# Optimization experiments

Hardware: AMD Instinct MI355X
Metric: run time of the kernel (lower is better)

Reference implementation:

```python
import jax, jax.numpy as jnp
import numpy as np
import math

D_MODEL = 512
N_HEADS = 8
FACTOR = 5
B, L = 2, 2048


def setup_inputs() -> dict:
    key = jax.random.key(0)
    ks = jax.random.split(key, 10)
    s = 1.0 / math.sqrt(D_MODEL)
    inp = {
        "x": jax.random.normal(ks[0], (B, L, D_MODEL), dtype=jnp.float32),
        "samp_idx": jax.random.randint(ks[1], (FACTOR * L,), 0, L),
        "Wq": jax.random.normal(ks[2], (D_MODEL, D_MODEL), dtype=jnp.float32) * s,
        "bq": jnp.zeros((D_MODEL,), dtype=jnp.float32),
        "Wk": jax.random.normal(ks[3], (D_MODEL, D_MODEL), dtype=jnp.float32) * s,
        "bk": jnp.zeros((D_MODEL,), dtype=jnp.float32),
        "Wv": jax.random.normal(ks[4], (D_MODEL, D_MODEL), dtype=jnp.float32) * s,
        "bv": jnp.zeros((D_MODEL,), dtype=jnp.float32),
        "Wo": jax.random.normal(ks[5], (D_MODEL, D_MODEL), dtype=jnp.float32) * s,
        "bo": jnp.zeros((D_MODEL,), dtype=jnp.float32),
    }
    return inp


def reference(x, Wq, bq, Wk, bk, Wv, bv, Wo, bo, samp_idx):
    B_, L_, D = x.shape
    H = N_HEADS
    dk = D // H
    scale = 1.0 / math.sqrt(dk)

    def proj(W, b):
        # torch Linear: x @ W.T + b, then split heads -> [B, H, L, dk]
        y = jnp.einsum('bld,ed->ble', x, W) + b
        return y.reshape(B_, L_, H, dk).transpose(0, 2, 1, 3)

    q = proj(Wq, bq)
    k = proj(Wk, bk)
    v = proj(Wv, bv)

    # _prob_QK: random key sampling (shared indices across B, H)
    K_sample = k[:, :, samp_idx, :]                       # [B, H, factor*L, dk]
    QKs = jnp.einsum('bhle,bhse->bhls', q, K_sample) * scale  # [B, H, L, factor*L]
    M = QKs.max(-1) - QKs.mean(-1)                        # [B, H, L]
    U = jnp.argmax(M, axis=-1)                            # [B, H] -- single query per head

    # gather the selected query per (b, h): [B, H, 1, dk]
    q_red = jnp.take_along_axis(q, U[:, :, None, None], axis=2)

    scores = jnp.einsum('bhle,bhse->bhls', q_red, k) * scale  # [B, H, 1, L]
    attn = jax.nn.softmax(scores, axis=-1)
    context = jnp.einsum('bhls,bhse->bhle', attn, v)          # [B, H, 1, dk]

    # expand to all query positions, merge heads
    context = jnp.broadcast_to(context, (B_, H, L_, dk))
    context = context.transpose(0, 2, 1, 3).reshape(B_, L_, D)
    return jnp.einsum('bld,ed->ble', context, Wo) + bo
```

## Files before the change

kernel.cpp:

```cpp
#include <hip/hip_runtime.h>

#define B_ 2
#define L_ 2048
#define D_ 512
#define H_ 8
#define DK 64
#define S_ 10240
#define SCALE 0.125f

#define QSZ (4096 * 512)

typedef _Float16 f16;
typedef __attribute__((ext_vector_type(8))) _Float16 f16x8;
typedef __attribute__((ext_vector_type(4))) float f32x4;

#define AS1 __attribute__((address_space(1)))
#define AS3 __attribute__((address_space(3)))

__global__ __launch_bounds__(256) void prep_kernel(
    const float* __restrict__ x,
    const float* __restrict__ Wq, const float* __restrict__ Wk,
    const float* __restrict__ bq, const float* __restrict__ bk,
    const int* __restrict__ samp,
    f16* __restrict__ xh, f16* __restrict__ xl,
    f16* __restrict__ wh, f16* __restrict__ wl,
    float* __restrict__ biascat, int* __restrict__ counts,
    float* __restrict__ xbc_part)
{
    const int bid = blockIdx.x;
    const int t = threadIdx.x;
    if (bid < 1024) {
        const size_t i0 = ((size_t)bid * 256 + t) * 8;
        const float4 a = *(const float4*)&x[i0];
        const float4 b = *(const float4*)&x[i0 + 4];
        const float vals[8] = {a.x, a.y, a.z, a.w, b.x, b.y, b.z, b.w};
        union { f16 h[8]; uint4 u; } H, Lo;
#pragma unroll
        for (int j = 0; j < 8; j++) {
            const f16 hh = (f16)vals[j];
            H.h[j] = hh;
            Lo.h[j] = (f16)(vals[j] - (float)hh);
        }
        *(uint4*)&xh[i0] = H.u;
        *(uint4*)&xl[i0] = Lo.u;
    } else if (bid < 1280) {
        const size_t i0 = ((size_t)(bid - 1024) * 256 + t) * 8;
        const float* src = (i0 < (size_t)512 * 512) ? Wq + i0
                                                    : Wk + (i0 - (size_t)512 * 512);
        const float4 a = *(const float4*)&src[0];
        const float4 b = *(const float4*)&src[4];
        const float vals[8] = {a.x, a.y, a.z, a.w, b.x, b.y, b.z, b.w};
        union { f16 h[8]; uint4 u; } H, Lo;
#pragma unroll
        for (int j = 0; j < 8; j++) {
            const f16 hh = (f16)vals[j];
            H.h[j] = hh;
            Lo.h[j] = (f16)(vals[j] - (float)hh);
        }
        *(uint4*)&wh[i0] = H.u;
        *(uint4*)&wl[i0] = Lo.u;
        if (bid == 1024)
            for (int e = t; e < 1024; e += 256)
                biascat[e] = (e < 512) ? bq[e] : bk[e - 512];
    } else if (bid < 1344) {
        const int p = bid - 1280;
        const int bb = p >> 5, chunk = p & 31;
        const int s0 = chunk * 320;
        float ax = 0.f, ay = 0.f;
        const float* xb = x + (size_t)bb * L_ * D_ + t * 2;
        for (int i = 0; i < 320; i++) {
            const int j = samp[s0 + i];
            const float2 v = *(const float2*)(xb + (size_t)j * D_);
            ax += v.x; ay += v.y;
        }
        float2 st; st.x = ax; st.y = ay;
        *(float2*)&xbc_part[((size_t)(bb * 32 + chunk)) * 512 + t * 2] = st;
    } else {
        int4 z; z.x = 0; z.y = 0; z.z = 0; z.w = 0;
        ((int4*)counts)[(bid - 1344) * 256 + t] = z;
    }
}

__global__ __launch_bounds__(256) void projqk_kernel(
    const f16* __restrict__ xh, const f16* __restrict__ xl,
    const f16* __restrict__ wh, const f16* __restrict__ wl,
    const float* __restrict__ biascat,
    const float* __restrict__ xbc_part, const float* __restrict__ Wk,
    const float* __restrict__ bk, const int* __restrict__ samp,
    int* __restrict__ counts, float* __restrict__ kbar,
    f16* __restrict__ qh, f16* __restrict__ ql,
    f16* __restrict__ kh, f16* __restrict__ kl)
{
    const int bid = blockIdx.x;
    const int t = threadIdx.x;

    __shared__ __align__(16) f16 lds[24576];

    if (bid >= 512) {
        const int bh = bid - 512;
        const int b = bh >> 3, h = bh & 7;
        float* xc = (float*)lds;

        for (int i = bh * 640 + t; i < (bh + 1) * 640; i += 256)
            atomicAdd(&counts[samp[i]], 1);

        float ax = 0.f, ay = 0.f;
#pragma unroll
        for (int p = 0; p < 32; p++) {
            const float2 v = *(const float2*)&xbc_part[((size_t)(b * 32 + p)) * 512 + t * 2];
            ax += v.x; ay += v.y;
        }
        xc[t * 2]     = ax * (1.0f / (float)S_);
        xc[t * 2 + 1] = ay * (1.0f / (float)S_);
        __syncthreads();

        const int row = t >> 2, quarter = t & 3;
        const float* wr = Wk + (size_t)(h * 64 + row) * 512 + quarter * 128;
        float s = 0.f;
#pragma unroll 8
        for (int d = 0; d < 32; d++) {
            const float4 w4 = *(const float4*)&wr[d * 4];
            const int xo = quarter * 128 + d * 4;
            s += w4.x * xc[xo] + w4.y * xc[xo + 1] + w4.z * xc[xo + 2] + w4.w * xc[xo + 3];
        }
        s += __shfl_xor(s, 1);
        s += __shfl_xor(s, 2);
        if (quarter == 0) kbar[bh * 64 + row] = s + bk[h * 64 + row];
        return;
    }

    const int n0 = (bid & 63) * 64;
    const int e0 = (bid >> 6) * 128;

    f16* ash = lds;
    f16* asl = lds + 4096;
    f16* bsh = lds + 8192;
    f16* bsl = lds + 16384;

    const int lane = t & 63, wid = t >> 6;
    const int wr = wid >> 1, wc = wid & 1;
    const int lrow = lane & 15, lk = lane >> 4;
    const int srw = lane >> 3;
    const int scg = (lane & 7) ^ srw;

    f32x4 acc[2][4];
#pragma unroll
    for (int i = 0; i < 2; i++)
#pragma unroll
        for (int j = 0; j < 4; j++)
#pragma unroll
            for (int r = 0; r < 4; r++) acc[i][j][r] = 0.f;

    for (int kt = 0; kt < 8; kt++) {
        __syncthreads();
#pragma unroll
        for (int i_ = 0; i_ < 2; i_++) {
            const int chunk = wid * 2 + i_;
            const int row = chunk * 8 + srw;
            const size_t goa = (size_t)(n0 + row) * 512 + kt * 64 + scg * 8;
            __builtin_amdgcn_global_load_lds((const AS1 void*)(xh + goa),
                                             (AS3 void*)(&ash[chunk * 512]), 16, 0, 0);
            __builtin_amdgcn_global_load_lds((const AS1 void*)(xl + goa),
                                             (AS3 void*)(&asl[chunk * 512]), 16, 0, 0);
        }
#pragma unroll
        for (int i_ = 0; i_ < 4; i_++) {
            const int chunk = wid * 4 + i_;
            const int row = chunk * 8 + srw;
            const size_t gob = (size_t)(e0 + row) * 512 + kt * 64 + scg * 8;
            __builtin_amdgcn_global_load_lds((const AS1 void*)(wh + gob),
                                             (AS3 void*)(&bsh[chunk * 512]), 16, 0, 0);
            __builtin_amdgcn_global_load_lds((const AS1 void*)(wl + gob),
                                             (AS3 void*)(&bsl[chunk * 512]), 16, 0, 0);
        }
        __syncthreads();

#pragma unroll
        for (int kk = 0; kk < 2; kk++) {
            f16x8 ah[2], al[2], bh_[4], bl_[4];
#pragma unroll
            for (int lt = 0; lt < 2; lt++) {
                const int row = wr * 32 + lt * 16 + lrow;
                const int cs = (kk * 4 + lk) ^ (row & 7);
                const int o = row * 64 + cs * 8;
                ah[lt] = *(const f16x8*)&ash[o];
                al[lt] = *(const f16x8*)&asl[o];
            }
#pragma unroll
            for (int jt = 0; jt < 4; jt++) {
                const int row = wc * 64 + jt * 16 + lrow;
                const int cs = (kk * 4 + lk) ^ (row & 7);
                const int o = row * 64 + cs * 8;
                bh_[jt] = *(const f16x8*)&bsh[o];
                bl_[jt] = *(const f16x8*)&bsl[o];
            }
#pragma unroll
            for (int lt = 0; lt < 2; lt++)
#pragma unroll
                for (int jt = 0; jt < 4; jt++) {
                    acc[lt][jt] = __builtin_amdgcn_mfma_f32_16x16x32_f16(
                        ah[lt], bh_[jt], acc[lt][jt], 0, 0, 0);
                    acc[lt][jt] = __builtin_amdgcn_mfma_f32_16x16x32_f16(
                        ah[lt], bl_[jt], acc[lt][jt], 0, 0, 0);
                    acc[lt][jt] = __builtin_amdgcn_mfma_f32_16x16x32_f16(
                        al[lt], bh_[jt], acc[lt][jt], 0, 0, 0);
                }
        }
    }

    const int PSTR = 72;
    f16* tile = lds + wid * 32 * PSTR;
    const int ebase = e0 + wc * 64;
    const bool isQ = ((bid >> 6) < 4);
    const int colbase = ((bid >> 6) & 3) * 128;

#pragma unroll
    for (int round = 0; round < 2; round++) {
        __syncthreads();
#pragma unroll
        for (int jt = 0; jt < 4; jt++) {
            const float bval = biascat[ebase + jt * 16 + lrow];
#pragma unroll
            for (int lt = 0; lt < 2; lt++)
#pragma unroll
                for (int r = 0; r < 4; r++) {
                    const float y = acc[lt][jt][r] + bval;
                    const f16 hi = (f16)y;
                    const f16 val = (round == 0) ? hi : (f16)(y - (float)hi);
                    tile[(lt * 16 + lk * 4 + r) * PSTR + jt * 16 + lrow] = val;
                }
        }
        __syncthreads();
        f16* dst = isQ ? ((round == 0) ? qh : ql) : ((round == 0) ? kh : kl);
        for (int i = t; i < 1024; i += 256) {
            const int row = i >> 4, cc = i & 15;
            const int swid = (row >> 5) * 2 + (cc >> 3);
            const int trow = row & 31, tcol = (cc & 7) * 8;
            const int n = n0 + row;
            const int col = colbase + cc * 8;
            *(uint4*)&dst[(size_t)n * 512 + col] =
                *(const uint4*)&lds[swid * 32 * PSTR + trow * PSTR + tcol];
        }
    }
}

__global__ __launch_bounds__(256, 2) void mstat_kernel(
    const f16* __restrict__ qh, const f16* __restrict__ ql,
    const f16* __restrict__ kh, const f16* __restrict__ kl,
    const int* __restrict__ counts, const float* __restrict__ kbar,
    float* __restrict__ bestv, int* __restrict__ besti)
{
    const int id = blockIdx.x;
    const int xcd = id & 7, seq = id >> 3;
    const int bh = xcd * 2 + (seq >> 5);
    const int inner = seq & 31;
    const int lt16 = inner >> 1;
    const int js = inner & 1;
    const int jbase = js * 8;
    const int b = bh >> 3, h = bh & 7;
    const int l0 = lt16 * 128;
    const int t = threadIdx.x;
    const int lane = t & 63, wid = t >> 6;
    const int wr = wid >> 1, wc = wid & 1;
    const int lrow = lane & 15, lk = lane >> 4;

    __shared__ __align__(16) f16 kbuf[2][2][128 * 64];
    __shared__ float kbar_lds[64];
    __shared__ float dot_lds[128];
    __shared__ float wv_[4];
    __shared__ int wi_[4];

    f16x8 qa_h[2][4], qa_l[2][4];
    {
        const size_t qrowbase = (size_t)(b * L_ + l0 + wr * 64) * D_ + h * DK;
#pragma unroll
        for (int kk = 0; kk < 2; kk++)
#pragma unroll
            for (int lt = 0; lt < 4; lt++) {
                const size_t o = qrowbase + (size_t)(lt * 16 + lrow) * D_ + kk * 32 + lk * 8;
                qa_h[kk][lt] = *(const f16x8*)&qh[o];
                qa_l[kk][lt] = *(const f16x8*)&ql[o];
            }
    }
    if (t < 64) kbar_lds[t] = kbar[bh * 64 + t];

    const f16* khb = kh + (size_t)b * L_ * D_ + h * DK;
    const f16* klb = kl + (size_t)b * L_ * D_ + h * DK;

    const int srw = lane >> 3;
    const int scg = (lane & 7) ^ srw;
#define STAGE_TILE(jt, nb)                                                     \
    {                                                                          \
        const size_t gb0 = (size_t)((jt) * 128) * D_;                          \
        _Pragma("unroll")                                                      \
        for (int i_ = 0; i_ < 4; i_++) {                                       \
            const int chunk = wid * 4 + i_;                                    \
            const size_t go = gb0 + (size_t)(chunk * 8 + srw) * D_ + scg * 8;  \
            __builtin_amdgcn_global_load_lds(                                  \
                (const AS1 void*)(khb + go),                                   \
                (AS3 void*)(&kbuf[nb][0][chunk * 512]), 16, 0, 0);             \
            __builtin_amdgcn_global_load_lds(                                  \
                (const AS1 void*)(klb + go),                                   \
                (AS3 void*)(&kbuf[nb][1][chunk * 512]), 16, 0, 0);             \
        }                                                                      \
    }

    STAGE_TILE(jbase, 0)
    __syncthreads();

    float rmax[4][4];
#pragma unroll
    for (int lt = 0; lt < 4; lt++)
#pragma unroll
        for (int r = 0; r < 4; r++) rmax[lt][r] = -3.9e38f;

    int cur = 0;
    for (int jj = 0; jj < 8; jj++) {
        const int jt = jbase + jj;
        if (jj < 7) STAGE_TILE(jt + 1, cur ^ 1)

        f32x4 acc[4][4];
#pragma unroll
        for (int i = 0; i < 4; i++)
#pragma unroll
            for (int j = 0; j < 4; j++)
#pragma unroll
                for (int r = 0; r < 4; r++) acc[i][j][r] = 0.f;

#pragma unroll
        for (int kk = 0; kk < 2; kk++) {
            f16x8 bhf[4], blf[4];
#pragma unroll
            for (int jtt = 0; jtt < 4; jtt++) {
                const int row = wc * 64 + jtt * 16 + lrow;
                const int cs = (kk * 4 + lk) ^ (row & 7);
                const int o = row * 64 + cs * 8;
                bhf[jtt] = *(const f16x8*)&kbuf[cur][0][o];
                blf[jtt] = *(const f16x8*)&kbuf[cur][1][o];
            }
#pragma unroll
            for (int lt = 0; lt < 4; lt++)
#pragma unroll
                for (int jtt = 0; jtt < 4; jtt++) {
                    acc[lt][jtt] = __builtin_amdgcn_mfma_f32_16x16x32_f16(
                        qa_h[kk][lt], bhf[jtt], acc[lt][jtt], 0, 0, 0);
                    acc[lt][jtt] = __builtin_amdgcn_mfma_f32_16x16x32_f16(
                        qa_h[kk][lt], blf[jtt], acc[lt][jtt], 0, 0, 0);
                    acc[lt][jtt] = __builtin_amdgcn_mfma_f32_16x16x32_f16(
                        qa_l[kk][lt], bhf[jtt], acc[lt][jtt], 0, 0, 0);
                }
        }

#pragma unroll
        for (int jtt = 0; jtt < 4; jtt++) {
            const int cj = jt * 128 + wc * 64 + jtt * 16 + lrow;
            const float addend = (counts[cj] > 0) ? 0.f : -3.0e38f;
#pragma unroll
            for (int lt = 0; lt < 4; lt++)
#pragma unroll
                for (int r = 0; r < 4; r++)
                    rmax[lt][r] = fmaxf(rmax[lt][r], acc[lt][jtt][r] + addend);
        }

        __syncthreads();
        cur ^= 1;
    }

#pragma unroll
    for (int m = 1; m < 16; m <<= 1)
#pragma unroll
        for (int lt = 0; lt < 4; lt++)
#pragma unroll
            for (int r = 0; r < 4; r++)
                rmax[lt][r] = fmaxf(rmax[lt][r], __shfl_xor(rmax[lt][r], m));

    {
        float dlt[4];
#pragma unroll
        for (int lt = 0; lt < 4; lt++) {
            float d = 0.f;
#pragma unroll
            for (int kk = 0; kk < 2; kk++) {
                const f16x8 hv = qa_h[kk][lt];
                const f16x8 lv = qa_l[kk][lt];
#pragma unroll
                for (int i = 0; i < 8; i++)
                    d += ((float)hv[i] + (float)lv[i]) * kbar_lds[kk * 32 + lk * 8 + i];
            }
            dlt[lt] = d;
        }
#pragma unroll
        for (int lt = 0; lt < 4; lt++) {
            dlt[lt] += __shfl_xor(dlt[lt], 16);
            dlt[lt] += __shfl_xor(dlt[lt], 32);
        }
        if (lane < 16) {
#pragma unroll
            for (int lt = 0; lt < 4; lt++)
                dot_lds[wr * 64 + lt * 16 + lane] = dlt[lt];
        }
    }
    __syncthreads();

    float bv_ = -3.9e38f;
    int bi_ = 0x7fffffff;
#pragma unroll
    for (int lt = 0; lt < 4; lt++)
#pragma unroll
        for (int r = 0; r < 4; r++) {
            const int rl_ = wr * 64 + lt * 16 + lk * 4 + r;
            const float val = rmax[lt][r] - dot_lds[rl_];
            const int idx = l0 + rl_;
            if (val > bv_ || (val == bv_ && idx < bi_)) { bv_ = val; bi_ = idx; }
        }
#pragma unroll
    for (int m = 1; m < 64; m <<= 1) {
        const float ov = __shfl_xor(bv_, m);
        const int oi = __shfl_xor(bi_, m);
        if (ov > bv_ || (ov == bv_ && oi < bi_)) { bv_ = ov; bi_ = oi; }
    }
    if (lane == 0) { wv_[wid] = bv_; wi_[wid] = bi_; }
    __syncthreads();
    if (t == 0) {
        float fb = wv_[0]; int fi = wi_[0];
#pragma unroll
        for (int w = 1; w < 4; w++) {
            if (wv_[w] > fb || (wv_[w] == fb && wi_[w] < fi)) { fb = wv_[w]; fi = wi_[w]; }
        }
        bestv[bh * 32 + lt16 * 2 + js] = fb;
        besti[bh * 32 + lt16 * 2 + js] = fi;
    }
#undef STAGE_TILE
}

__global__ __launch_bounds__(256) void ctx_part_kernel(
    const f16* __restrict__ qh, const f16* __restrict__ ql,
    const f16* __restrict__ kh, const f16* __restrict__ kl,
    const float* __restrict__ x,
    const float* __restrict__ bestv, const int* __restrict__ besti,
    float* __restrict__ xbar_part, float* __restrict__ cm, float* __restrict__ cs)
{
    const int c = blockIdx.x;
    const int b = blockIdx.y;
    const int l0 = c * 16;
    const int t = threadIdx.x;

    __shared__ float qr[8][64];
    __shared__ float w[8][16];
    __shared__ int u_lds[8];

    if (t < 8) {
        const int bh = b * 8 + t;
        float best = -3.9e38f; int bi = 0x7fffffff;
        for (int cc = 0; cc < 32; cc++) {
            const float v = bestv[bh * 32 + cc];
            const int oi = besti[bh * 32 + cc];
            if (v > best || (v == best && oi < bi)) { best = v; bi = oi; }
        }
        u_lds[t] = bi;
    }
    __syncthreads();

    {
        const int h = t >> 5, i2 = (t & 31) * 2;
        const int u = u_lds[h];
        const size_t o = (size_t)(b * L_ + u) * D_ + h * DK + i2;
        qr[h][i2]     = (float)qh[o]     + (float)ql[o];
        qr[h][i2 + 1] = (float)qh[o + 1] + (float)ql[o + 1];
    }
    __syncthreads();

    {
        const int dotid = t >> 1, half = t & 1;
        const int row = dotid & 15, h = dotid >> 4;
        const size_t off = (size_t)(b * L_ + l0 + row) * D_ + h * DK + half * 32;
        const f16* krh = kh + off;
        const f16* krl = kl + off;
        float dot = 0.f;
#pragma unroll
        for (int cc = 0; cc < 4; cc++) {
            const f16x8 hv = *(const f16x8*)&krh[cc * 8];
            const f16x8 lv = *(const f16x8*)&krl[cc * 8];
#pragma unroll
            for (int i = 0; i < 8; i++)
                dot += ((float)hv[i] + (float)lv[i]) * qr[h][half * 32 + cc * 8 + i];
        }
        dot += __shfl_xor(dot, 1);
        if (half == 0) w[h][row] = dot * SCALE;
    }
    __syncthreads();

    if (t < 8) {
        float m = w[t][0];
#pragma unroll
        for (int i = 1; i < 16; i++) m = fmaxf(m, w[t][i]);
        float s = 0.f;
#pragma unroll
        for (int i = 0; i < 16; i++) {
            const float e = expf(w[t][i] - m);
            w[t][i] = e;
            s += e;
        }
        cm[(size_t)(b * 8 + t) * 128 + c] = m;
        cs[(size_t)(b * 8 + t) * 128 + c] = s;
    }
    __syncthreads();

    {
        float ax[8], ay[8];
#pragma unroll
        for (int h = 0; h < 8; h++) { ax[h] = 0.f; ay[h] = 0.f; }
        const float* xb = x + (size_t)(b * L_ + l0) * D_ + t * 2;
#pragma unroll
        for (int i = 0; i < 16; i++) {
            const float2 xv = *(const float2*)(xb + (size_t)i * D_);
#pragma unroll
            for (int h = 0; h < 8; h++) {
                ax[h] = fmaf(w[h][i], xv.x, ax[h]);
                ay[h] = fmaf(w[h][i], xv.y, ay[h]);
            }
        }
#pragma unroll
        for (int h = 0; h < 8; h++) {
            float2 st; st.x = ax[h]; st.y = ay[h];
            *(float2*)&xbar_part[((size_t)(b * 8 + h) * 128 + c) * 512 + t * 2] = st;
        }
    }
}

__global__ __launch_bounds__(256) void ctx_combine_kernel(
    const float* __restrict__ xbar_part, const float* __restrict__ cm,
    const float* __restrict__ cs, const float* __restrict__ Wv,
    const float* __restrict__ bv, float* __restrict__ ctx)
{
    const int bh = blockIdx.x;
    const int h = bh & 7;
    const int t = threadIdx.x;
    __shared__ float xbar[512];

    float M = -3.9e38f;
    for (int cc = 0; cc < 128; cc++) M = fmaxf(M, cm[(size_t)bh * 128 + cc]);
    float denom = 0.f, ax = 0.f, ay = 0.f;
    for (int cc = 0; cc < 128; cc++) {
        const float f = expf(cm[(size_t)bh * 128 + cc] - M);
        denom += f * cs[(size_t)bh * 128 + cc];
        const float2 p = *(const float2*)
            &xbar_part[((size_t)bh * 128 + cc) * 512 + t * 2];
        ax = fmaf(f, p.x, ax);
        ay = fmaf(f, p.y, ay);
    }
    xbar[t * 2] = ax; xbar[t * 2 + 1] = ay;
    __syncthreads();

    if (t < 64) {
        const float* wr = Wv + (size_t)(h * 64 + t) * D_;
        float acc = 0.f;
#pragma unroll 8
        for (int d = 0; d < 128; d++) {
            const float4 wv4 = *(const float4*)&wr[d * 4];
            acc += wv4.x * xbar[d * 4] + wv4.y * xbar[d * 4 + 1] +
                   wv4.z * xbar[d * 4 + 2] + wv4.w * xbar[d * 4 + 3];
        }
        ctx[bh * 64 + t] = acc / denom + bv[h * 64 + t];
    }
}

__global__ __launch_bounds__(256) void out_kernel(
    const float* __restrict__ ctx, const float* __restrict__ Wo,
    const float* __restrict__ bo, float* __restrict__ out)
{
    const int b = blockIdx.x;
    const int sl = blockIdx.y;
    const int t = threadIdx.x;
    __shared__ float cb[512];
    __shared__ float row[512];

    cb[t] = ctx[b * 512 + t];
    cb[t + 256] = ctx[b * 512 + 256 + t];
    __syncthreads();

#pragma unroll
    for (int r = 0; r < 2; r++) {
        const int e = t + r * 256;
        const float* wr = Wo + (size_t)e * D_;
        float acc = 0.f;
#pragma unroll 8
        for (int c = 0; c < 128; c++) {
            const float4 wv = *(const float4*)(wr + c * 4);
            acc += wv.x * cb[c * 4] + wv.y * cb[c * 4 + 1] +
                   wv.z * cb[c * 4 + 2] + wv.w * cb[c * 4 + 3];
        }
        row[e] = acc + bo[e];
    }
    __syncthreads();

    const float4* r4 = (const float4*)row;
    float4* o4 = (float4*)(out + ((size_t)b * L_ + sl * 32) * D_);
    for (int i = t; i < 32 * 128; i += 256) {
        const int l = i >> 7, c = i & 127;
        o4[l * 128 + c] = r4[c];
    }
}

extern "C" void kernel_launch(void* const* d_in, const int* in_sizes, int n_in,
                              void* d_out, int out_size, void* d_ws, size_t ws_size,
                              hipStream_t stream)
{
    const float* x   = (const float*)d_in[0];
    const int* samp  = (const int*)d_in[1];
    const float* Wq  = (const float*)d_in[2];
    const float* bq  = (const float*)d_in[3];
    const float* Wk  = (const float*)d_in[4];
    const float* bk  = (const float*)d_in[5];
    const float* Wv  = (const float*)d_in[6];
    const float* bv  = (const float*)d_in[7];
    const float* Wo  = (const float*)d_in[8];
    const float* bo  = (const float*)d_in[9];
    float* out = (float*)d_out;

    f16* qh = (f16*)d_ws;
    f16* ql = qh + QSZ;
    f16* kh = ql + QSZ;
    f16* kl = kh + QSZ;
    f16* xh = kl + QSZ;
    f16* xl = xh + QSZ;
    f16* wh = xl + QSZ;
    f16* wl = wh + 1024 * 512;
    float* fbase     = (float*)(wl + 1024 * 512);
    float* biascat   = fbase;
    float* xbc_part  = biascat + 1024;
    float* xbar_part = xbc_part + 32768;
    float* cm        = xbar_part + 1048576;
    float* cs        = cm + 2048;
    float* bestv     = cs + 2048;
    float* kbar      = bestv + 512;
    float* ctx       = kbar + 1024;
    int* counts      = (int*)(ctx + 1024);
    int* besti       = counts + 2048;

    prep_kernel<<<1346, 256, 0, stream>>>(x, Wq, Wk, bq, bk, samp,
                                          xh, xl, wh, wl, biascat, counts,
                                          xbc_part);
    projqk_kernel<<<528, 256, 0, stream>>>(xh, xl, wh, wl, biascat,
                                           xbc_part, Wk, bk, samp, counts, kbar,
                                           qh, ql, kh, kl);
    mstat_kernel<<<512, 256, 0, stream>>>(qh, ql, kh, kl, counts, kbar,
                                          bestv, besti);
    ctx_part_kernel<<<dim3(128, 2), 256, 0, stream>>>(qh, ql, kh, kl, x,
                                                      bestv, besti,
                                                      xbar_part, cm, cs);
    ctx_combine_kernel<<<16, 256, 0, stream>>>(xbar_part, cm, cs, Wv, bv, ctx);
    out_kernel<<<dim3(2, 64), 256, 0, stream>>>(ctx, Wo, bo, out);
}
```

Baseline: 143.1 us.

## Fuse fp16 hi/lo split into projection GEMM and build sample mask per block

```diff
diff --git a/kernel.cpp b/kernel.cpp
--- a/kernel.cpp
+++ b/kernel.cpp
@@ -17,92 +17,55 @@
 #define AS1 __attribute__((address_space(1)))
 #define AS3 __attribute__((address_space(3)))
 
+__device__ __forceinline__ void split44(const float4 a, const float4 b,
+                                        f16x8& hi, f16x8& lo)
+{
+    const float v[8] = {a.x, a.y, a.z, a.w, b.x, b.y, b.z, b.w};
+#pragma unroll
+    for (int i = 0; i < 8; i++) {
+        const f16 h = (f16)v[i];
+        hi[i] = h;
+        lo[i] = (f16)(v[i] - (float)h);
+    }
+}
+
 __global__ __launch_bounds__(256) void prep_kernel(
+    const float* __restrict__ x, const int* __restrict__ samp,
+    float* __restrict__ xbc_part)
+{
+    const int p = blockIdx.x;
+    const int t = threadIdx.x;
+    const int bb = p >> 5, chunk = p & 31;
+    const int s0 = chunk * 320;
+    float ax = 0.f, ay = 0.f;
+    const float* xb = x + (size_t)bb * L_ * D_ + t * 2;
+    for (int i = 0; i < 320; i++) {
+        const int j = samp[s0 + i];
+        const float2 v = *(const float2*)(xb + (size_t)j * D_);
+        ax += v.x; ay += v.y;
+    }
+    float2 st; st.x = ax; st.y = ay;
+    *(float2*)&xbc_part[((size_t)(bb * 32 + chunk)) * 512 + t * 2] = st;
+}
+
+__global__ __launch_bounds__(256) void projqk_kernel(
     const float* __restrict__ x,
     const float* __restrict__ Wq, const float* __restrict__ Wk,
     const float* __restrict__ bq, const float* __restrict__ bk,
-    const int* __restrict__ samp,
-    f16* __restrict__ xh, f16* __restrict__ xl,
-    f16* __restrict__ wh, f16* __restrict__ wl,
-    float* __restrict__ biascat, int* __restrict__ counts,
-    float* __restrict__ xbc_part)
+    const float* __restrict__ xbc_part,
+    float* __restrict__ kbar,
+    f16* __restrict__ qh, f16* __restrict__ ql,
+    f16* __restrict__ kh, f16* __restrict__ kl)
 {
     const int bid = blockIdx.x;
     const int t = threadIdx.x;
-    if (bid < 1024) {
-        const size_t i0 = ((size_t)bid * 256 + t) * 8;
-        const float4 a = *(const float4*)&x[i0];
-        const float4 b = *(const float4*)&x[i0 + 4];
-        const float vals[8] = {a.x, a.y, a.z, a.w, b.x, b.y, b.z, b.w};
-        union { f16 h[8]; uint4 u; } H, Lo;
-#pragma unroll
-        for (int j = 0; j < 8; j++) {
-            const f16 hh = (f16)vals[j];
-            H.h[j] = hh;
-            Lo.h[j] = (f16)(vals[j] - (float)hh);
-        }
-        *(uint4*)&xh[i0] = H.u;
-        *(uint4*)&xl[i0] = Lo.u;
-    } else if (bid < 1280) {
-        const size_t i0 = ((size_t)(bid - 1024) * 256 + t) * 8;
-        const float* src = (i0 < (size_t)512 * 512) ? Wq + i0
-                                                    : Wk + (i0 - (size_t)512 * 512);
-        const float4 a = *(const float4*)&src[0];
-        const float4 b = *(const float4*)&src[4];
-        const float vals[8] = {a.x, a.y, a.z, a.w, b.x, b.y, b.z, b.w};
-        union { f16 h[8]; uint4 u; } H, Lo;
-#pragma unroll
-        for (int j = 0; j < 8; j++) {
-            const f16 hh = (f16)vals[j];
-            H.h[j] = hh;
-            Lo.h[j] = (f16)(vals[j] - (float)hh);
-        }
-        *(uint4*)&wh[i0] = H.u;
-        *(uint4*)&wl[i0] = Lo.u;
-        if (bid == 1024)
-            for (int e = t; e < 1024; e += 256)
-                biascat[e] = (e < 512) ? bq[e] : bk[e - 512];
-    } else if (bid < 1344) {
-        const int p = bid - 1280;
-        const int bb = p >> 5, chunk = p & 31;
-        const int s0 = chunk * 320;
-        float ax = 0.f, ay = 0.f;
-        const float* xb = x + (size_t)bb * L_ * D_ + t * 2;
-        for (int i = 0; i < 320; i++) {
-            const int j = samp[s0 + i];
-            const float2 v = *(const float2*)(xb + (size_t)j * D_);
-            ax += v.x; ay += v.y;
-        }
-        float2 st; st.x = ax; st.y = ay;
-        *(float2*)&xbc_part[((size_t)(bb * 32 + chunk)) * 512 + t * 2] = st;
-    } else {
-        int4 z; z.x = 0; z.y = 0; z.z = 0; z.w = 0;
-        ((int4*)counts)[(bid - 1344) * 256 + t] = z;
-    }
-}
-
-__global__ __launch_bounds__(256) void projqk_kernel(
-    const f16* __restrict__ xh, const f16* __restrict__ xl,
-    const f16* __restrict__ wh, const f16* __restrict__ wl,
-    const float* __restrict__ biascat,
-    const float* __restrict__ xbc_part, const float* __restrict__ Wk,
-    const float* __restrict__ bk, const int* __restrict__ samp,
-    int* __restrict__ counts, float* __restrict__ kbar,
-    f16* __restrict__ qh, f16* __restrict__ ql,
-    f16* __restrict__ kh, f16* __restrict__ kl)
-{
-    const int bid = blockIdx.x;
-    const int t = threadIdx.x;
-
-    __shared__ __align__(16) f16 lds[24576];
+
+    __shared__ __align__(16) float lds[12288];
 
     if (bid >= 512) {
         const int bh = bid - 512;
         const int b = bh >> 3, h = bh & 7;
-        float* xc = (float*)lds;
-
-        for (int i = bh * 640 + t; i < (bh + 1) * 640; i += 256)
-            atomicAdd(&counts[samp[i]], 1);
+        float* xc = lds;
 
         float ax = 0.f, ay = 0.f;
 #pragma unroll
@@ -131,17 +94,16 @@
 
     const int n0 = (bid & 63) * 64;
     const int e0 = (bid >> 6) * 128;
-
-    f16* ash = lds;
-    f16* asl = lds + 4096;
-    f16* bsh = lds + 8192;
-    f16* bsl = lds + 16384;
+    const bool isQ = ((bid >> 6) < 4);
+    const float* Wsrc = isQ ? Wq : Wk;
+    const int wrow0 = isQ ? e0 : (e0 - 512);
+
+    float* Af = lds;
+    float* Bf = lds + 4096;
 
     const int lane = t & 63, wid = t >> 6;
     const int wr = wid >> 1, wc = wid & 1;
     const int lrow = lane & 15, lk = lane >> 4;
-    const int srw = lane >> 3;
-    const int scg = (lane & 7) ^ srw;
 
     f32x4 acc[2][4];
 #pragma unroll
@@ -154,64 +116,64 @@
     for (int kt = 0; kt < 8; kt++) {
         __syncthreads();
 #pragma unroll
-        for (int i_ = 0; i_ < 2; i_++) {
-            const int chunk = wid * 2 + i_;
-            const int row = chunk * 8 + srw;
-            const size_t goa = (size_t)(n0 + row) * 512 + kt * 64 + scg * 8;
-            __builtin_amdgcn_global_load_lds((const AS1 void*)(xh + goa),
-                                             (AS3 void*)(&ash[chunk * 512]), 16, 0, 0);
-            __builtin_amdgcn_global_load_lds((const AS1 void*)(xl + goa),
-                                             (AS3 void*)(&asl[chunk * 512]), 16, 0, 0);
-        }
-#pragma unroll
         for (int i_ = 0; i_ < 4; i_++) {
-            const int chunk = wid * 4 + i_;
-            const int row = chunk * 8 + srw;
-            const size_t gob = (size_t)(e0 + row) * 512 + kt * 64 + scg * 8;
-            __builtin_amdgcn_global_load_lds((const AS1 void*)(wh + gob),
-                                             (AS3 void*)(&bsh[chunk * 512]), 16, 0, 0);
-            __builtin_amdgcn_global_load_lds((const AS1 void*)(wl + gob),
-                                             (AS3 void*)(&bsl[chunk * 512]), 16, 0, 0);
+            const int L = wid * 256 + i_ * 64 + lane;
+            const int row = L >> 4, c16 = L & 15;
+            const int g16 = c16 ^ (row & 7);
+            const size_t go = (size_t)(n0 + row) * 512 + kt * 64 + g16 * 4;
+            __builtin_amdgcn_global_load_lds((const AS1 void*)(x + go),
+                                             (AS3 void*)(&Af[L * 4]), 16, 0, 0);
+        }
+#pragma unroll
+        for (int i_ = 0; i_ < 8; i_++) {
+            const int L = wid * 512 + i_ * 64 + lane;
+            const int row = L >> 4, c16 = L & 15;
+            const int g16 = c16 ^ (row & 7);
+            const size_t go = (size_t)(wrow0 + row) * 512 + kt * 64 + g16 * 4;
+            __builtin_amdgcn_global_load_lds((const AS1 void*)(Wsrc + go),
+                                             (AS3 void*)(&Bf[L * 4]), 16, 0, 0);
         }
         __syncthreads();
 
 #pragma unroll
         for (int kk = 0; kk < 2; kk++) {
-            f16x8 ah[2], al[2], bh_[4], bl_[4];
+            f16x8 ah[2], al[2], bhf[4], blf[4];
 #pragma unroll
             for (int lt = 0; lt < 2; lt++) {
                 const int row = wr * 32 + lt * 16 + lrow;
-                const int cs = (kk * 4 + lk) ^ (row & 7);
-                const int o = row * 64 + cs * 8;
-                ah[lt] = *(const f16x8*)&ash[o];
-                al[lt] = *(const f16x8*)&asl[o];
+                const int c2 = kk * 4 + lk;
+                const int base = row * 64;
+                const float4 f0 = *(const float4*)&Af[base + (((c2 * 2)     ^ (row & 7)) << 2)];
+                const float4 f1 = *(const float4*)&Af[base + (((c2 * 2 + 1) ^ (row & 7)) << 2)];
+                split44(f0, f1, ah[lt], al[lt]);
             }
 #pragma unroll
             for (int jt = 0; jt < 4; jt++) {
                 const int row = wc * 64 + jt * 16 + lrow;
-                const int cs = (kk * 4 + lk) ^ (row & 7);
-                const int o = row * 64 + cs * 8;
-                bh_[jt] = *(const f16x8*)&bsh[o];
-                bl_[jt] = *(const f16x8*)&bsl[o];
+                const int c2 = kk * 4 + lk;
+                const int base = row * 64;
+                const float4 f0 = *(const float4*)&Bf[base + (((c2 * 2)     ^ (row & 7)) << 2)];
+                const float4 f1 = *(const float4*)&Bf[base + (((c2 * 2 + 1) ^ (row & 7)) << 2)];
+                split44(f0, f1, bhf[jt], blf[jt]);
             }
 #pragma unroll
             for (int lt = 0; lt < 2; lt++)
 #pragma unroll
                 for (int jt = 0; jt < 4; jt++) {
                     acc[lt][jt] = __builtin_amdgcn_mfma_f32_16x16x32_f16(
-                        ah[lt], bh_[jt], acc[lt][jt], 0, 0, 0);
+                        ah[lt], bhf[jt], acc[lt][jt], 0, 0, 0);
                     acc[lt][jt] = __builtin_amdgcn_mfma_f32_16x16x32_f16(
-                        ah[lt], bl_[jt], acc[lt][jt], 0, 0, 0);
+                        ah[lt], blf[jt], acc[lt][jt], 0, 0, 0);
                     acc[lt][jt] = __builtin_amdgcn_mfma_f32_16x16x32_f16(
-                        al[lt], bh_[jt], acc[lt][jt], 0, 0, 0);
+                        al[lt], bhf[jt], acc[lt][jt], 0, 0, 0);
                 }
         }
     }
 
     const int PSTR = 72;
-    f16* tile = lds + wid * 32 * PSTR;
-    const int ebase = e0 + wc * 64;
-    const bool isQ = ((bid >> 6) < 4);
+    f16* tile = (f16*)lds + wid * 32 * PSTR;
+    const int ebaseL = (isQ ? e0 : e0 - 512) + wc * 64;
+    const float* bsrc = isQ ? bq : bk;
     const int colbase = ((bid >> 6) & 3) * 128;
 
 #pragma unroll
@@ -219,7 +181,7 @@
         __syncthreads();
 #pragma unroll
         for (int jt = 0; jt < 4; jt++) {
-            const float bval = biascat[ebase + jt * 16 + lrow];
+            const float bval = bsrc[ebaseL + jt * 16 + lrow];
 #pragma unroll
             for (int lt = 0; lt < 2; lt++)
 #pragma unroll
@@ -239,7 +201,7 @@
             const int n = n0 + row;
             const int col = colbase + cc * 8;
             *(uint4*)&dst[(size_t)n * 512 + col] =
-                *(const uint4*)&lds[swid * 32 * PSTR + trow * PSTR + tcol];
+                *(const uint4*)&((const f16*)lds)[swid * 32 * PSTR + trow * PSTR + tcol];
         }
     }
 }
@@ -247,7 +209,7 @@
 __global__ __launch_bounds__(256, 2) void mstat_kernel(
     const f16* __restrict__ qh, const f16* __restrict__ ql,
     const f16* __restrict__ kh, const f16* __restrict__ kl,
-    const int* __restrict__ counts, const float* __restrict__ kbar,
+    const int* __restrict__ samp, const float* __restrict__ kbar,
     float* __restrict__ bestv, int* __restrict__ besti)
 {
     const int id = blockIdx.x;
@@ -265,6 +227,7 @@
     const int lrow = lane & 15, lk = lane >> 4;
 
     __shared__ __align__(16) f16 kbuf[2][2][128 * 64];
+    __shared__ unsigned char msk[1024];
     __shared__ float kbar_lds[64];
     __shared__ float dot_lds[128];
     __shared__ float wv_[4];
@@ -283,6 +246,7 @@
             }
     }
     if (t < 64) kbar_lds[t] = kbar[bh * 64 + t];
+    ((int*)msk)[t] = 0;
 
     const f16* khb = kh + (size_t)b * L_ * D_ + h * DK;
     const f16* klb = kl + (size_t)b * L_ * D_ + h * DK;
@@ -308,6 +272,15 @@
     STAGE_TILE(jbase, 0)
     __syncthreads();
 
+    {
+        const int j0g = js * 1024;
+        for (int i = t; i < S_; i += 256) {
+            const unsigned d = (unsigned)(samp[i] - j0g);
+            if (d < 1024u) msk[d] = 1;
+        }
+    }
+    __syncthreads();
+
     float rmax[4][4];
 #pragma unroll
     for (int lt = 0; lt < 4; lt++)
@@ -353,8 +326,8 @@
 
 #pragma unroll
         for (int jtt = 0; jtt < 4; jtt++) {
-            const int cj = jt * 128 + wc * 64 + jtt * 16 + lrow;
-            const float addend = (counts[cj] > 0) ? 0.f : -3.0e38f;
+            const int cjl = jj * 128 + wc * 64 + jtt * 16 + lrow;
+            const float addend = msk[cjl] ? 0.f : -3.0e38f;
 #pragma unroll
             for (int lt = 0; lt < 4; lt++)
 #pragma unroll
@@ -622,29 +595,20 @@
     f16* ql = qh + QSZ;
     f16* kh = ql + QSZ;
     f16* kl = kh + QSZ;
-    f16* xh = kl + QSZ;
-    f16* xl = xh + QSZ;
-    f16* wh = xl + QSZ;
-    f16* wl = wh + 1024 * 512;
-    float* fbase     = (float*)(wl + 1024 * 512);
-    float* biascat   = fbase;
-    float* xbc_part  = biascat + 1024;
+    float* fbase     = (float*)(kl + QSZ);
+    float* xbc_part  = fbase;
     float* xbar_part = xbc_part + 32768;
     float* cm        = xbar_part + 1048576;
     float* cs        = cm + 2048;
     float* bestv     = cs + 2048;
     float* kbar      = bestv + 512;
     float* ctx       = kbar + 1024;
-    int* counts      = (int*)(ctx + 1024);
-    int* besti       = counts + 2048;
-
-    prep_kernel<<<1346, 256, 0, stream>>>(x, Wq, Wk, bq, bk, samp,
-                                          xh, xl, wh, wl, biascat, counts,
-                                          xbc_part);
-    projqk_kernel<<<528, 256, 0, stream>>>(xh, xl, wh, wl, biascat,
-                                           xbc_part, Wk, bk, samp, counts, kbar,
+    int* besti       = (int*)(ctx + 1024);
+
+    prep_kernel<<<64, 256, 0, stream>>>(x, samp, xbc_part);
+    projqk_kernel<<<528, 256, 0, stream>>>(x, Wq, Wk, bq, bk, xbc_part, kbar,
                                            qh, ql, kh, kl);
-    mstat_kernel<<<512, 256, 0, stream>>>(qh, ql, kh, kl, counts, kbar,
+    mstat_kernel<<<512, 256, 0, stream>>>(qh, ql, kh, kl, samp, kbar,
                                           bestv, besti);
     ctx_part_kernel<<<dim3(128, 2), 256, 0, stream>>>(qh, ql, kh, kl, x,
                                                       bestv, besti,
```

Measured after the change: 152.0 us. 1.06x slower.
